# Performance work log

Measured on AMD Instinct MI355X. Metric: run time of the kernel, lower is better.

Reference implementation:

```python
import jax, jax.numpy as jnp
import numpy as np

SCALING = 16.0  # lora_alpha
R = 16


def setup_inputs() -> dict:
    key = jax.random.key(0)
    ks = jax.random.split(key, 6)
    B, S, D_IN, D_OUT = 4, 2048, 4096, 4096
    x = jax.random.normal(ks[0], (B, S, D_IN), dtype=jnp.float32)
    W = jax.random.normal(ks[1], (D_OUT, D_IN), dtype=jnp.float32) * 0.02
    b = jax.random.normal(ks[2], (D_OUT,), dtype=jnp.float32) * 0.02
    lora_A = jax.random.normal(ks[3], (R, D_IN), dtype=jnp.float32) * 0.02
    lora_B = jax.random.normal(ks[4], (D_OUT, R), dtype=jnp.float32) * 0.02
    lora_c = jax.random.uniform(ks[5], (R, 1), dtype=jnp.float32)
    return {"x": x, "W": W, "b": b, "lora_A": lora_A, "lora_B": lora_B, "lora_c": lora_c}


def reference(x, W, b, lora_A, lora_B, lora_c):
    # Base (quantized-in-torch, dense here) linear: x @ W.T + b
    result = jnp.einsum("bsi,oi->bso", x, W) + b
    # LoRA correction: x @ (A * c).T @ B.T * scaling / r
    # Contract down to rank-r first to avoid a [D_IN, D_OUT] intermediate.
    A_scaled = lora_A * lora_c                       # [r, D_IN]
    h = jnp.einsum("bsi,ri->bsr", x, A_scaled)       # [B, S, r] (small)
    lora_out = jnp.einsum("bsr,or->bso", h, lora_B) * (SCALING / R)
    return result + lora_out
```

## Files before the change

### kernel.cpp

```cpp
#include <hip/hip_runtime.h>
#include <hip/hip_bf16.h>
#include <stdint.h>
#include <stddef.h>

#define D_IN   4096
#define D_OUT  4096
#define M_TOT  8192
#define R_RANK 16
#define LORA_SCALE 1.0f

typedef __attribute__((ext_vector_type(8))) short short8;
typedef __attribute__((ext_vector_type(4))) short short4v;
typedef __attribute__((ext_vector_type(4))) float f32x4;

#define GL2LDS16(g, l)                                                  \
  __builtin_amdgcn_global_load_lds(                                     \
      (const __attribute__((address_space(1))) void*)(g),               \
      (__attribute__((address_space(3))) void*)(l), 16, 0, 0)

__global__ __launch_bounds__(256) void prep_w(
    const float* __restrict__ W, const float* __restrict__ A,
    const float* __restrict__ c, const float* __restrict__ B,
    __hip_bfloat16* __restrict__ Wp) {
  int t  = threadIdx.x;
  int i  = blockIdx.x * 1024 + t * 4;
  int o0 = blockIdx.y * 4;

  float4 a4[R_RANK];
#pragma unroll
  for (int r = 0; r < R_RANK; r++) {
    float4 v = *(const float4*)(A + r * D_IN + i);
    float cr = c[r] * LORA_SCALE;
    v.x *= cr; v.y *= cr; v.z *= cr; v.w *= cr;
    a4[r] = v;
  }
#pragma unroll
  for (int oo = 0; oo < 4; oo++) {
    int o = o0 + oo;
    float4 w = *(const float4*)(W + (size_t)o * D_IN + i);
#pragma unroll
    for (int r = 0; r < R_RANK; r++) {
      float br = B[o * R_RANK + r];
      w.x += br * a4[r].x; w.y += br * a4[r].y;
      w.z += br * a4[r].z; w.w += br * a4[r].w;
    }
    __hip_bfloat16 tb[4];
    tb[0] = __float2bfloat16(w.x); tb[1] = __float2bfloat16(w.y);
    tb[2] = __float2bfloat16(w.z); tb[3] = __float2bfloat16(w.w);
    *(short4v*)(Wp + (size_t)o * D_IN + i) = *(const short4v*)tb;
  }
}

__global__ __launch_bounds__(256) void pack_x(
    const float* __restrict__ x, __hip_bfloat16* __restrict__ Xp) {
  size_t idx = ((size_t)blockIdx.x * 256 + threadIdx.x) * 8;
  float4 v0 = *(const float4*)(x + idx);
  float4 v1 = *(const float4*)(x + idx + 4);
  __hip_bfloat16 t[8];
  t[0] = __float2bfloat16(v0.x); t[1] = __float2bfloat16(v0.y);
  t[2] = __float2bfloat16(v0.z); t[3] = __float2bfloat16(v0.w);
  t[4] = __float2bfloat16(v1.x); t[5] = __float2bfloat16(v1.y);
  t[6] = __float2bfloat16(v1.z); t[7] = __float2bfloat16(v1.w);
  *(short8*)(Xp + idx) = *(const short8*)t;
}

#define BM 128
#define BN 128
#define BK 64

__global__ __launch_bounds__(256) void gemm_main(
    const __hip_bfloat16* __restrict__ Xp,
    const __hip_bfloat16* __restrict__ Wp,
    const float* __restrict__ bias,
    float* __restrict__ out) {
  __shared__ __align__(16) __hip_bfloat16 As[BM * BK];
  __shared__ __align__(16) __hip_bfloat16 Bs[BN * BK];

  int tid  = threadIdx.x;
  int wid  = tid >> 6;
  int lane = tid & 63;
  int wm = wid >> 1, wn = wid & 1;
  int m0 = blockIdx.y * BM;
  int n0 = blockIdx.x * BN;
  int l15 = lane & 15;
  int kg  = lane >> 4;
  int rx  = l15 & 7;

  int srow  = lane >> 3;
  int ldcol = (lane & 7) * 8;
  int gcol  = ((lane & 7) ^ srow) * 8;

  f32x4 acc[4][4];
#pragma unroll
  for (int i = 0; i < 4; i++)
#pragma unroll
    for (int j = 0; j < 4; j++) acc[i][j] = (f32x4){0.f, 0.f, 0.f, 0.f};

  for (int kt = 0; kt < D_IN; kt += BK) {
    __syncthreads();
#pragma unroll
    for (int j = 0; j < 4; j++) {
      int row = wid * 32 + j * 8 + srow;
      const __hip_bfloat16* ga = Xp + (size_t)(m0 + row) * D_IN + kt + gcol;
      GL2LDS16(ga, As + row * BK + ldcol);
      const __hip_bfloat16* gb = Wp + (size_t)(n0 + row) * D_IN + kt + gcol;
      GL2LDS16(gb, Bs + row * BK + ldcol);
    }
    __syncthreads();

#pragma unroll
    for (int kk = 0; kk < BK; kk += 32) {
      int ck = (kk >> 3) + kg;
      int pc = (ck ^ rx) * 8;
      short8 af[4], bb[4];
#pragma unroll
      for (int am = 0; am < 4; am++)
        af[am] = *(const short8*)(As + (wm * 64 + am * 16 + l15) * BK + pc);
#pragma unroll
      for (int bn = 0; bn < 4; bn++)
        bb[bn] = *(const short8*)(Bs + (wn * 64 + bn * 16 + l15) * BK + pc);
#pragma unroll
      for (int am = 0; am < 4; am++)
#pragma unroll
        for (int bn = 0; bn < 4; bn++)
          acc[am][bn] = __builtin_amdgcn_mfma_f32_16x16x32_bf16(
              af[am], bb[bn], acc[am][bn], 0, 0, 0);
    }
  }

  float bv[4];
#pragma unroll
  for (int bn = 0; bn < 4; bn++) bv[bn] = bias[n0 + wn * 64 + bn * 16 + l15];
#pragma unroll
  for (int am = 0; am < 4; am++) {
#pragma unroll
    for (int reg = 0; reg < 4; reg++) {
      int row = m0 + wm * 64 + am * 16 + kg * 4 + reg;
      float* po = out + (size_t)row * D_OUT + n0 + wn * 64 + l15;
#pragma unroll
      for (int bn = 0; bn < 4; bn++) po[bn * 16] = acc[am][bn][reg] + bv[bn];
    }
  }
}

extern "C" void kernel_launch(void* const* d_in, const int* in_sizes, int n_in,
                              void* d_out, int out_size, void* d_ws, size_t ws_size,
                              hipStream_t stream) {
  const float* x  = (const float*)d_in[0];
  const float* W  = (const float*)d_in[1];
  const float* b  = (const float*)d_in[2];
  const float* lA = (const float*)d_in[3];
  const float* lB = (const float*)d_in[4];
  const float* lc = (const float*)d_in[5];
  float* out = (float*)d_out;

  char* ws = (char*)d_ws;
  __hip_bfloat16* Xp = (__hip_bfloat16*)ws;
  __hip_bfloat16* Wp = (__hip_bfloat16*)(ws + (size_t)67108864);

  pack_x<<<dim3(M_TOT * D_IN / (256 * 8)), dim3(256), 0, stream>>>(x, Xp);
  prep_w<<<dim3(D_IN / 1024, D_OUT / 4), dim3(256), 0, stream>>>(W, lA, lc, lB, Wp);
  gemm_main<<<dim3(D_OUT / BN, M_TOT / BM), dim3(256), 0, stream>>>(Xp, Wp, b, out);
}
```

Before: 603.1 us.

## Replace GEMM with 256x256-tile double-buffered pipelined kernel using 8 waves

Replaces the single-buffered 128x128 GEMM with a 256x256 tile kernel of 512 threads that double-buffers LDS and splits each K tile into halves. Global-to-LDS loads for the next tile are interleaved with MFMA work, using explicit vmcnt waits, soft barriers and s_setprio around the MFMA bursts. The goal is to hide load latency and raise arithmetic intensity per block. In exchange it needs 128KB of LDS per block and a large accumulator register footprint, which limits occupancy, and the hand-placed waitcnt and barriers must be correct to avoid read hazards.

```diff
diff --git a/kernel.cpp b/kernel.cpp
--- a/kernel.cpp
+++ b/kernel.cpp
@@ -64,81 +64,140 @@
   *(short8*)(Xp + idx) = *(const short8*)t;
 }
 
-#define BM 128
-#define BN 128
 #define BK 64
-
-__global__ __launch_bounds__(256) void gemm_main(
+#define NT (D_IN / BK)
+
+#define SOFF(BUFI, AB, KH) ((((BUFI) * 2 + (AB)) * 2 + (KH)) * 8192)
+
+#define VMCNT(N) asm volatile("s_waitcnt vmcnt(" #N ")" ::: "memory")
+#define HARD_BARRIER() asm volatile("s_barrier" ::: "memory")
+#define SOFT_BARRIER() __builtin_amdgcn_s_barrier()
+
+#define STAGE_HALF(BUFI, AB, KH, TS)                                         \
+  do {                                                                       \
+    const __hip_bfloat16* _src = (AB) ? Wp : Xp;                             \
+    const int _rb = (AB) ? n0 : m0;                                          \
+    const int _kb = (TS) * BK + (KH) * 32;                                   \
+    _Pragma("unroll")                                                        \
+    for (int _is = 0; _is < 2; ++_is) {                                      \
+      const int _p = _is * 512 + tid;                     \
+      const int _row = _p >> 2;                                              \
+      const int _c = (_p & 3) ^ ((_row >> 1) & 3);      \
+      GL2LDS16(_src + (size_t)(_rb + _row) * D_IN + _kb + _c * 8,            \
+               smem + SOFF(BUFI, AB, KH) + _p * 8);                          \
+    }                                                                        \
+  } while (0)
+
+#define LOAD_AF(BUFI, KH, MH)                                                \
+  _Pragma("unroll")                                                          \
+  for (int _j = 0; _j < 4; ++_j)                                             \
+    af[_j] = *(const short8*)(smem + SOFF(BUFI, 0, KH) +                     \
+                              (wm * 128 + ((MH) * 4 + _j) * 16 + l15) * 32 + \
+                              cph * 8);
+
+#define LOAD_BF(BUFI, KH)                                                    \
+  _Pragma("unroll")                                                          \
+  for (int _nn = 0; _nn < 4; ++_nn)                                          \
+    bf[_nn] = *(const short8*)(smem + SOFF(BUFI, 1, KH) +                    \
+                               (wn * 64 + _nn * 16 + l15) * 32 + cph * 8);
+
+#define MFMA_HALF(MH)                                                        \
+  do {                                                                       \
+    __builtin_amdgcn_s_setprio(1);                                           \
+    _Pragma("unroll")                                                        \
+    for (int _j = 0; _j < 4; ++_j)                                           \
+      _Pragma("unroll")                                                      \
+      for (int _nn = 0; _nn < 4; ++_nn)                                      \
+        acc[(MH) * 4 + _j][_nn] = __builtin_amdgcn_mfma_f32_16x16x32_bf16(   \
+            af[_j], bf[_nn], acc[(MH) * 4 + _j][_nn], 0, 0, 0);              \
+    __builtin_amdgcn_s_setprio(0);                                           \
+  } while (0)
+
+#define TILE_BODY(BUFI, NBUF, T, DO_STAGE)                                   \
+  do {                                                                       \
+                                                        \
+    LOAD_AF(BUFI, 0, 0);                                                     \
+    LOAD_BF(BUFI, 0);                                                        \
+    if (DO_STAGE) STAGE_HALF(NBUF, 0, 0, (T) + 1);                           \
+    SOFT_BARRIER();                                                          \
+    MFMA_HALF(0);                                                            \
+    SOFT_BARRIER();                                                          \
+                                                        \
+    LOAD_AF(BUFI, 0, 1);                                                     \
+    if (DO_STAGE) STAGE_HALF(NBUF, 1, 0, (T) + 1);                           \
+    SOFT_BARRIER();                                                          \
+    MFMA_HALF(1);                                                            \
+    if (DO_STAGE) { VMCNT(4); } else { VMCNT(0); }                           \
+    HARD_BARRIER();                                                          \
+                                                        \
+    LOAD_AF(BUFI, 1, 0);                                                     \
+    LOAD_BF(BUFI, 1);                                                        \
+    if (DO_STAGE) STAGE_HALF(NBUF, 0, 1, (T) + 1);                           \
+    SOFT_BARRIER();                                                          \
+    MFMA_HALF(0);                                                            \
+    SOFT_BARRIER();                                                          \
+                                                        \
+    LOAD_AF(BUFI, 1, 1);                                                     \
+    if (DO_STAGE) STAGE_HALF(NBUF, 1, 1, (T) + 1);                           \
+    SOFT_BARRIER();                                                          \
+    MFMA_HALF(1);                                                            \
+    if (DO_STAGE) { VMCNT(4); } else { VMCNT(0); }                           \
+    HARD_BARRIER();                                                          \
+  } while (0)
+
+__global__ __launch_bounds__(512, 2) void gemm_256(
     const __hip_bfloat16* __restrict__ Xp,
     const __hip_bfloat16* __restrict__ Wp,
     const float* __restrict__ bias,
     float* __restrict__ out) {
-  __shared__ __align__(16) __hip_bfloat16 As[BM * BK];
-  __shared__ __align__(16) __hip_bfloat16 Bs[BN * BK];
-
-  int tid  = threadIdx.x;
-  int wid  = tid >> 6;
-  int lane = tid & 63;
-  int wm = wid >> 1, wn = wid & 1;
-  int m0 = blockIdx.y * BM;
-  int n0 = blockIdx.x * BN;
-  int l15 = lane & 15;
-  int kg  = lane >> 4;
-  int rx  = l15 & 7;
-
-  int srow  = lane >> 3;
-  int ldcol = (lane & 7) * 8;
-  int gcol  = ((lane & 7) ^ srow) * 8;
-
-  f32x4 acc[4][4];
-#pragma unroll
-  for (int i = 0; i < 4; i++)
+  __shared__ __align__(16) __hip_bfloat16 smem[2 * 2 * 2 * 8192];
+
+  const int tid  = threadIdx.x;
+  const int wid  = tid >> 6;
+  const int lane = tid & 63;
+  const int wm = wid >> 2;
+  const int wn = wid & 3;
+  const int l15 = lane & 15;
+  const int kg  = lane >> 4;
+  const int cph = kg ^ ((l15 >> 1) & 3);
+  const int m0 = blockIdx.y * 256;
+  const int n0 = blockIdx.x * 256;
+
+  f32x4 acc[8][4];
+#pragma unroll
+  for (int i = 0; i < 8; i++)
 #pragma unroll
     for (int j = 0; j < 4; j++) acc[i][j] = (f32x4){0.f, 0.f, 0.f, 0.f};
 
-  for (int kt = 0; kt < D_IN; kt += BK) {
-    __syncthreads();
-#pragma unroll
-    for (int j = 0; j < 4; j++) {
-      int row = wid * 32 + j * 8 + srow;
-      const __hip_bfloat16* ga = Xp + (size_t)(m0 + row) * D_IN + kt + gcol;
-      GL2LDS16(ga, As + row * BK + ldcol);
-      const __hip_bfloat16* gb = Wp + (size_t)(n0 + row) * D_IN + kt + gcol;
-      GL2LDS16(gb, Bs + row * BK + ldcol);
-    }
-    __syncthreads();
-
-#pragma unroll
-    for (int kk = 0; kk < BK; kk += 32) {
-      int ck = (kk >> 3) + kg;
-      int pc = (ck ^ rx) * 8;
-      short8 af[4], bb[4];
-#pragma unroll
-      for (int am = 0; am < 4; am++)
-        af[am] = *(const short8*)(As + (wm * 64 + am * 16 + l15) * BK + pc);
-#pragma unroll
-      for (int bn = 0; bn < 4; bn++)
-        bb[bn] = *(const short8*)(Bs + (wn * 64 + bn * 16 + l15) * BK + pc);
-#pragma unroll
-      for (int am = 0; am < 4; am++)
-#pragma unroll
-        for (int bn = 0; bn < 4; bn++)
-          acc[am][bn] = __builtin_amdgcn_mfma_f32_16x16x32_bf16(
-              af[am], bb[bn], acc[am][bn], 0, 0, 0);
-    }
-  }
+  short8 af[4];
+  short8 bf[4];
+
+  STAGE_HALF(0, 0, 0, 0);
+  STAGE_HALF(0, 1, 0, 0);
+  STAGE_HALF(0, 0, 1, 0);
+  STAGE_HALF(0, 1, 1, 0);
+  VMCNT(4);
+  HARD_BARRIER();
+
+#pragma unroll 1
+  for (int t = 0; t < NT - 2; t += 2) {
+    TILE_BODY(0, 1, t, 1);
+    TILE_BODY(1, 0, t + 1, 1);
+  }
+  TILE_BODY(0, 1, NT - 2, 1);
+  TILE_BODY(1, 0, NT - 1, 0);
 
   float bv[4];
 #pragma unroll
-  for (int bn = 0; bn < 4; bn++) bv[bn] = bias[n0 + wn * 64 + bn * 16 + l15];
-#pragma unroll
-  for (int am = 0; am < 4; am++) {
-#pragma unroll
-    for (int reg = 0; reg < 4; reg++) {
-      int row = m0 + wm * 64 + am * 16 + kg * 4 + reg;
+  for (int nn = 0; nn < 4; ++nn) bv[nn] = bias[n0 + wn * 64 + nn * 16 + l15];
+#pragma unroll
+  for (int mm = 0; mm < 8; ++mm) {
+#pragma unroll
+    for (int reg = 0; reg < 4; ++reg) {
+      const int row = m0 + wm * 128 + mm * 16 + kg * 4 + reg;
       float* po = out + (size_t)row * D_OUT + n0 + wn * 64 + l15;
 #pragma unroll
-      for (int bn = 0; bn < 4; bn++) po[bn * 16] = acc[am][bn][reg] + bv[bn];
+      for (int nn = 0; nn < 4; ++nn) po[nn * 16] = acc[mm][nn][reg] + bv[nn];
     }
   }
 }
@@ -160,5 +219,5 @@
 
   pack_x<<<dim3(M_TOT * D_IN / (256 * 8)), dim3(256), 0, stream>>>(x, Xp);
   prep_w<<<dim3(D_IN / 1024, D_OUT / 4), dim3(256), 0, stream>>>(W, lA, lc, lB, Wp);
-  gemm_main<<<dim3(D_OUT / BN, M_TOT / BM), dim3(256), 0, stream>>>(Xp, Wp, b, out);
-}
+  gemm_256<<<dim3(D_OUT / 256, M_TOT / 256), dim3(512), 0, stream>>>(Xp, Wp, b, out);
+}
```

Result: faster. 501.3 us (-16.9%).
